# Kernel tuning notes

Hardware: AMD Instinct MI355X
Metric: run time of the kernel (lower is better)

The kernel has to match this reference:

```python
import jax, jax.numpy as jnp
import numpy as np

N = 524288
E = 16          # embedding_dim
R = 128         # dense grid resolution
H = 128         # hidden_dim
W0_SIREN = 30.0


def trilinear(grid, p):
    """grid: [R,R,R,E]; p: [N,3] in [0,1]. Returns [N,E]."""
    r = grid.shape[0]
    x = p * (r - 1)
    i0 = jnp.clip(jnp.floor(x), 0, r - 2).astype(jnp.int32)   # [N,3]
    f = x - i0.astype(x.dtype)                                # [N,3] fractional
    gf = grid.reshape(-1, grid.shape[-1])                     # [R^3, E]
    out = jnp.zeros((p.shape[0], grid.shape[-1]), dtype=grid.dtype)
    for dx in (0, 1):
        wx = f[:, 0] if dx else (1.0 - f[:, 0])
        for dy in (0, 1):
            wy = f[:, 1] if dy else (1.0 - f[:, 1])
            for dz in (0, 1):
                wz = f[:, 2] if dz else (1.0 - f[:, 2])
                idx = (i0[:, 0] + dx) * r * r + (i0[:, 1] + dy) * r + (i0[:, 2] + dz)
                out = out + gf[idx] * (wx * wy * wz)[:, None]
    return out


def siren(h, W0, b0, W1, b1, Wo, bo):
    h = jnp.sin(W0_SIREN * (h @ W0.T + b0))
    h = jnp.sin(W0_SIREN * (h @ W1.T + b1))
    return h @ Wo.T + bo   # [N,1]


def setup_inputs() -> dict:
    key = jax.random.key(0)
    ks = jax.random.split(key, 8)
    positions = jax.random.uniform(ks[0], (N, 3), dtype=jnp.float32)  # in [0,1)
    grid = jax.random.uniform(ks[1], (R, R, R, E), jnp.float32, -1e-4, 1e-4)
    din = E + 3
    c0 = float(np.sqrt(6.0 / din) / W0_SIREN)
    c1 = float(np.sqrt(6.0 / H) / W0_SIREN)
    W0 = jax.random.uniform(ks[2], (H, din), jnp.float32, -c0, c0)
    b0 = jax.random.uniform(ks[3], (H,), jnp.float32, -c0, c0)
    W1 = jax.random.uniform(ks[4], (H, H), jnp.float32, -c1, c1)
    b1 = jax.random.uniform(ks[5], (H,), jnp.float32, -c1, c1)
    Wo = jax.random.uniform(ks[6], (1, H), jnp.float32, -c1, c1)
    bo = jax.random.uniform(ks[7], (1,), jnp.float32, -c1, c1)
    return {"positions": positions, "grid": grid, "W0": W0, "b0": b0,
            "W1": W1, "b1": b1, "Wo": Wo, "bo": bo}


def reference(positions, grid, W0, b0, W1, b1, Wo, bo):
    # torch code rebinds positions = positions*0.5+0.5 BEFORE autograd.grad,
    # so the eikonal gradient is w.r.t. the transformed coordinates p.
    p = positions * 0.5 + 0.5

    def sdf_fn(pp):
        emb = trilinear(grid, pp)
        return siren(jnp.concatenate([emb, pp], axis=-1), W0, b0, W1, b1, Wo, bo)

    sdf, vjp_fn = jax.vjp(sdf_fn, p)
    (grad_x,) = vjp_fn(jnp.ones_like(sdf))
    return sdf, grad_x
```

## Files before the change

kernel.cpp:

```cpp
#include <hip/hip_runtime.h>
#include <math.h>

#define NPTS 524288
#define EDIM 16
#define RES  128
#define HDIM 128
#define DIN  19
#define OXs  (RES*RES*EDIM)
#define OYs  (RES*EDIM)
#define OZs  (EDIM)
#define NBLK 256
#define NWAVE 12
#define BATCH (NWAVE * 16)
#define NITER 11

typedef _Float16 f16;
typedef __attribute__((ext_vector_type(8))) _Float16 f16x8;
typedef __attribute__((ext_vector_type(4))) float f32x4;

#define WS_P1 0
#define WS_P2 32768
#define WS_P0 65536
#define WS_P3 73728
#define WS_T  81920
#define WS_BYTES 84992

#define DS_ORDER() asm volatile("" ::: "memory")

__global__ void pack_weights(const float* __restrict__ W0, const float* __restrict__ b0,
                             const float* __restrict__ W1, const float* __restrict__ b1,
                             const float* __restrict__ Wo, unsigned char* __restrict__ ws) {
    int idx = blockIdx.x * 256 + threadIdx.x;
    f16* p1 = (f16*)(ws + WS_P1);
    f16* p2 = (f16*)(ws + WS_P2);
    f16* p0 = (f16*)(ws + WS_P0);
    f16* p3 = (f16*)(ws + WS_P3);
    float* tb = (float*)(ws + WS_T);
    if (idx < 16384) {
        int e = idx & 7, l = (idx >> 3) & 63, t = (idx >> 9) & 3, nt = idx >> 11;
        int c = l & 15, g = l >> 4;
        p1[idx] = (f16)W1[(c + 16*nt)*HDIM + (8*g + e + 32*t)];
    } else if (idx < 32768) {
        int i = idx - 16384;
        int e = i & 7, l = (i >> 3) & 63, t = (i >> 9) & 3, nt = i >> 11;
        int c = l & 15, g = l >> 4;
        p2[i] = (f16)W1[(8*g + e + 32*t)*HDIM + (c + 16*nt)];
    } else if (idx < 36864) {
        int i = idx - 32768;
        int e = i & 7, l = (i >> 3) & 63, nt = i >> 9;
        int c = l & 15, g = l >> 4;
        int d = 8*g + e;
        p0[i] = (d < EDIM) ? (f16)W0[(c + 16*nt)*DIN + d] : (f16)0.f;
    } else if (idx < 40960) {
        int i = idx - 36864;
        int e = i & 7, l = (i >> 3) & 63, t = (i >> 9) & 3, nt = i >> 11;
        int c = l & 15, g = l >> 4;
        int din = c + 16*nt;
        p3[i] = (din < DIN) ? (f16)W0[(8*g + e + 32*t)*DIN + din] : (f16)0.f;
    } else if (idx < 41728) {
        int i = idx - 40960;
        int j = i & 127, sel = i >> 7;
        float v;
        if (sel == 0)      v = W0[j*DIN + 16];
        else if (sel == 1) v = W0[j*DIN + 17];
        else if (sel == 2) v = W0[j*DIN + 18];
        else if (sel == 3) v = b0[j];
        else if (sel == 4) v = b1[j];
        else               v = Wo[j];
        tb[i] = v;
    }
}

__global__ __launch_bounds__(768, 1)
void sdf_mfma(const float* __restrict__ pos,
              const float* __restrict__ gridp,
              const unsigned char* __restrict__ ws,
              const float* __restrict__ bo,
              float* __restrict__ out) {
    __shared__ f16 sP1[16384];
    __shared__ f16 sP2[16384];
    __shared__ f16 sP0[4096];
    __shared__ f16 sP3[4096];
    __shared__ float sT[768];
    __shared__ unsigned char sBounce[NWAVE][4352];

    const int tid = threadIdx.x;
    {
        const uint4* src = (const uint4*)ws;
        uint4* d1 = (uint4*)sP1;
        uint4* d2 = (uint4*)sP2;
        uint4* d0 = (uint4*)sP0;
        uint4* d3 = (uint4*)sP3;
        uint4* dt = (uint4*)sT;
#pragma unroll
        for (int i = 0; i < 3; ++i) {
            int k = tid + i * 768;
            if (k < 2048) { d1[k] = src[k]; d2[k] = src[2048 + k]; }
        }
        if (tid < 512) { d0[tid] = src[4096 + tid]; d3[tid] = src[4608 + tid]; }
        if (tid < 192) dt[tid] = src[5120 + tid];
    }
    __syncthreads();

    const int l = tid & 63, w = tid >> 6;
    const int c = l & 15, g = l >> 4;
    const int s = g & 1, q = g >> 1;

    f16* sBW = (f16*)sBounce[w];
    const f16x8* P0 = (const f16x8*)sP0;
    const f16x8* P1 = (const f16x8*)sP1;
    const f16x8* P2 = (const f16x8*)sP2;
    const f16x8* P3 = (const f16x8*)sP3;
    const f32x4 z4 = {0.f, 0.f, 0.f, 0.f};
    const float bov = bo[0];

#pragma unroll 1
    for (int it = 0; it < NITER; ++it) {
        const int pbase = (blockIdx.x * NITER + it) * BATCH + w * 16;
        if (pbase >= NPTS) continue;
        const int pt = pbase + c;

        const float px = fmaf(pos[3*pt+0], 0.5f, 0.5f);
        const float py = fmaf(pos[3*pt+1], 0.5f, 0.5f);
        const float pz = fmaf(pos[3*pt+2], 0.5f, 0.5f);
        const float x0 = px*127.f, x1 = py*127.f, x2 = pz*127.f;
        int i0 = (int)floorf(x0); i0 = i0 < 0 ? 0 : (i0 > 126 ? 126 : i0);
        int i1 = (int)floorf(x1); i1 = i1 < 0 ? 0 : (i1 > 126 ? 126 : i1);
        int i2 = (int)floorf(x2); i2 = i2 < 0 ? 0 : (i2 > 126 ? 126 : i2);
        const float f0 = x0 - (float)i0, f1 = x1 - (float)i1, f2 = x2 - (float)i2;
        const float wx1 = f0, wx0 = 1.f - f0;
        const float wy1 = f1, wy0 = 1.f - f1;
        const float wz1 = f2, wz0 = 1.f - f2;
        const float* gb = gridp + (size_t)((i0*RES + i1)*RES + i2)*EDIM;

        float w8[8] = {0.f,0.f,0.f,0.f,0.f,0.f,0.f,0.f};
        {
            const float wxq = q ? wx1 : wx0;
#pragma unroll
            for (int j = 0; j < 4; ++j) {
                const float* gp = gb + q*OXs + ((j>>1)&1)*OYs + (j&1)*OZs + 8*s;
                float4 qa = *(const float4*)gp;
                float4 qb = *(const float4*)(gp + 4);
                const float wc = wxq * ((j&2)?wy1:wy0) * ((j&1)?wz1:wz0);
                w8[0] = fmaf(wc, qa.x, w8[0]);  w8[1] = fmaf(wc, qa.y, w8[1]);
                w8[2] = fmaf(wc, qa.z, w8[2]);  w8[3] = fmaf(wc, qa.w, w8[3]);
                w8[4] = fmaf(wc, qb.x, w8[4]);  w8[5] = fmaf(wc, qb.y, w8[5]);
                w8[6] = fmaf(wc, qb.z, w8[6]);  w8[7] = fmaf(wc, qb.w, w8[7]);
            }
        }
        f16x8 afe;
#pragma unroll
        for (int m = 0; m < 8; ++m) {
            const float full = w8[m] + __shfl_xor(w8[m], 32);
            afe[m] = (g < 2) ? (f16)full : (f16)0.f;
        }

        f32x4 acc[8];
        __builtin_amdgcn_s_setprio(1);
#pragma unroll
        for (int nt = 0; nt < 8; ++nt)
            acc[nt] = __builtin_amdgcn_mfma_f32_16x16x32_f16(afe, P0[nt*64 + l], z4, 0, 0, 0);
        __builtin_amdgcn_s_setprio(0);

        float rpx[4], rpy[4], rpz[4];
        {
            const float* pp = pos + 3 * (pbase + 4*g);
            const float4 fa = *(const float4*)(pp + 0);
            const float4 fb = *(const float4*)(pp + 4);
            const float4 fc = *(const float4*)(pp + 8);
            rpx[0] = fmaf(fa.x, 0.5f, 0.5f); rpy[0] = fmaf(fa.y, 0.5f, 0.5f); rpz[0] = fmaf(fa.z, 0.5f, 0.5f);
            rpx[1] = fmaf(fa.w, 0.5f, 0.5f); rpy[1] = fmaf(fb.x, 0.5f, 0.5f); rpz[1] = fmaf(fb.y, 0.5f, 0.5f);
            rpx[2] = fmaf(fb.z, 0.5f, 0.5f); rpy[2] = fmaf(fb.w, 0.5f, 0.5f); rpz[2] = fmaf(fc.x, 0.5f, 0.5f);
            rpx[3] = fmaf(fc.y, 0.5f, 0.5f); rpy[3] = fmaf(fc.z, 0.5f, 0.5f); rpz[3] = fmaf(fc.w, 0.5f, 0.5f);
        }
        float t0a[8][4];
#pragma unroll
        for (int nt = 0; nt < 8; ++nt) {
            const int j = c + 16*nt;
            const float t16 = sT[j], t17 = sT[128+j], t18 = sT[256+j], tb0 = sT[384+j];
#pragma unroll
            for (int r = 0; r < 4; ++r) {
                float a0 = acc[nt][r] + tb0;
                a0 = fmaf(rpx[r], t16, a0);
                a0 = fmaf(rpy[r], t17, a0);
                a0 = fmaf(rpz[r], t18, a0);
                const float t0 = 30.f * a0;
                t0a[nt][r] = t0;
                sBW[(4*g + r)*136 + j] = (f16)__sinf(t0);
            }
        }
        DS_ORDER();

        f16x8 af[4];
#pragma unroll
        for (int t = 0; t < 4; ++t)
            af[t] = *(const f16x8*)&sBW[c*136 + 32*t + 8*g];
        __builtin_amdgcn_s_setprio(1);
#pragma unroll
        for (int nt = 0; nt < 8; ++nt) {
            f32x4 a = z4;
#pragma unroll
            for (int t = 0; t < 4; ++t)
                a = __builtin_amdgcn_mfma_f32_16x16x32_f16(af[t], P1[(nt*4+t)*64 + l], a, 0, 0, 0);
            acc[nt] = a;
        }
        __builtin_amdgcn_s_setprio(0);

        float sp[4] = {0.f, 0.f, 0.f, 0.f};
#pragma unroll
        for (int nt = 0; nt < 8; ++nt) {
            const int j = c + 16*nt;
            const float b1j = sT[512+j], woj = sT[640+j];
#pragma unroll
            for (int r = 0; r < 4; ++r) {
                const float t1 = 30.f * (acc[nt][r] + b1j);
                sp[r] = fmaf(woj, __sinf(t1), sp[r]);
                sBW[(4*g + r)*136 + j] = (f16)(30.f * woj * __cosf(t1));
            }
        }
#pragma unroll
        for (int r = 0; r < 4; ++r) {
            sp[r] += __shfl_xor(sp[r], 1);
            sp[r] += __shfl_xor(sp[r], 2);
            sp[r] += __shfl_xor(sp[r], 4);
            sp[r] += __shfl_xor(sp[r], 8);
        }
        if (c == 0) {
#pragma unroll
            for (int r = 0; r < 4; ++r) out[pbase + 4*g + r] = sp[r] + bov;
        }
        DS_ORDER();

        float4 ca[2][4];
#pragma unroll
        for (int h = 0; h < 2; ++h) {
            const int cr = 2*g + h;
            const float* gp = gb + ((cr>>2)&1)*OXs + ((cr>>1)&1)*OYs + (cr&1)*OZs;
            ca[h][0] = *(const float4*)gp;
            ca[h][1] = *(const float4*)(gp + 4);
            ca[h][2] = *(const float4*)(gp + 8);
            ca[h][3] = *(const float4*)(gp + 12);
        }

#pragma unroll
        for (int t = 0; t < 4; ++t)
            af[t] = *(const f16x8*)&sBW[c*136 + 32*t + 8*g];
        __builtin_amdgcn_s_setprio(1);
#pragma unroll
        for (int nt = 0; nt < 8; ++nt) {
            f32x4 a = z4;
#pragma unroll
            for (int t = 0; t < 4; ++t)
                a = __builtin_amdgcn_mfma_f32_16x16x32_f16(af[t], P2[(nt*4+t)*64 + l], a, 0, 0, 0);
            acc[nt] = a;
        }
        __builtin_amdgcn_s_setprio(0);

#pragma unroll
        for (int nt = 0; nt < 8; ++nt) {
            const int k = c + 16*nt;
#pragma unroll
            for (int r = 0; r < 4; ++r) {
                const float da0 = acc[nt][r] * (30.f * __cosf(t0a[nt][r]));
                sBW[(4*g + r)*136 + k] = (f16)da0;
            }
        }
        DS_ORDER();

#pragma unroll
        for (int t = 0; t < 4; ++t)
            af[t] = *(const f16x8*)&sBW[c*136 + 32*t + 8*g];
        f32x4 d3a = z4, d3b = z4;
        __builtin_amdgcn_s_setprio(1);
#pragma unroll
        for (int t = 0; t < 4; ++t) {
            d3a = __builtin_amdgcn_mfma_f32_16x16x32_f16(af[t], P3[t*64 + l],     d3a, 0, 0, 0);
            d3b = __builtin_amdgcn_mfma_f32_16x16x32_f16(af[t], P3[(4+t)*64 + l], d3b, 0, 0, 0);
        }
        __builtin_amdgcn_s_setprio(0);

        float* sDV = (float*)sBounce[w];
#pragma unroll
        for (int r = 0; r < 4; ++r) sDV[(4*g + r)*20 + c] = d3a[r];
        if (c < 3) {
#pragma unroll
            for (int r = 0; r < 4; ++r) sDV[(4*g + r)*20 + 16 + c] = d3b[r];
        }
        DS_ORDER();

        const f32x4 dva = *(const f32x4*)&sDV[c*20 + 0];
        const f32x4 dvb = *(const f32x4*)&sDV[c*20 + 4];
        const f32x4 dvc = *(const f32x4*)&sDV[c*20 + 8];
        const f32x4 dvd = *(const f32x4*)&sDV[c*20 + 12];
        float scv[2];
#pragma unroll
        for (int h = 0; h < 2; ++h) {
            float sdot = ca[h][0].x*dva[0] + ca[h][0].y*dva[1] + ca[h][0].z*dva[2] + ca[h][0].w*dva[3]
                       + ca[h][1].x*dvb[0] + ca[h][1].y*dvb[1] + ca[h][1].z*dvb[2] + ca[h][1].w*dvb[3]
                       + ca[h][2].x*dvc[0] + ca[h][2].y*dvc[1] + ca[h][2].z*dvc[2] + ca[h][2].w*dvc[3]
                       + ca[h][3].x*dvd[0] + ca[h][3].y*dvd[1] + ca[h][3].z*dvd[2] + ca[h][3].w*dvd[3];
            scv[h] = sdot;
        }
        float* sSC = (float*)sBounce[w] + 320;
        sSC[c*8 + 2*g]     = scv[0];
        sSC[c*8 + 2*g + 1] = scv[1];
        DS_ORDER();
        if (g == 0) {
            const float* scp = &sSC[c*8];
            const float sc0 = scp[0], sc1 = scp[1], sc2 = scp[2], sc3 = scp[3];
            const float sc4 = scp[4], sc5 = scp[5], sc6 = scp[6], sc7 = scp[7];
            const float gx = 127.f * (wy0*wz0*(sc4-sc0) + wy0*wz1*(sc5-sc1) +
                                      wy1*wz0*(sc6-sc2) + wy1*wz1*(sc7-sc3));
            const float gy = 127.f * (wx0*wz0*(sc2-sc0) + wx0*wz1*(sc3-sc1) +
                                      wx1*wz0*(sc6-sc4) + wx1*wz1*(sc7-sc5));
            const float gz = 127.f * (wx0*wy0*(sc1-sc0) + wx0*wy1*(sc3-sc2) +
                                      wx1*wy0*(sc5-sc4) + wx1*wy1*(sc7-sc6));
            out[NPTS + 3*pt + 0] = gx + sDV[c*20 + 16];
            out[NPTS + 3*pt + 1] = gy + sDV[c*20 + 17];
            out[NPTS + 3*pt + 2] = gz + sDV[c*20 + 18];
        }
        DS_ORDER();
    }
}

#define JCHUNK 64
__global__ void transpose_w1(const float* __restrict__ W1, float* __restrict__ W1T) {
    int idx = blockIdx.x * 256 + threadIdx.x;
    if (idx < HDIM * HDIM) {
        int j = idx >> 7, k = idx & 127;
        W1T[k * HDIM + j] = W1[j * HDIM + k];
    }
}
#define LOAD16(gq)                                   \
    float4 q0 = *(const float4*)((gq) + 0);          \
    float4 q1 = *(const float4*)((gq) + 4);          \
    float4 q2 = *(const float4*)((gq) + 8);          \
    float4 q3 = *(const float4*)((gq) + 12);

template<int RS, int CS>
__global__ __launch_bounds__(256, 2)
void sdf_fused(const float* __restrict__ pos, const float* __restrict__ gridp,
               const float* __restrict__ W0, const float* __restrict__ b0,
               const float* __restrict__ W1m, const float* __restrict__ b1,
               const float* __restrict__ Wo, const float* __restrict__ bo,
               float* __restrict__ out) {
    const int i = blockIdx.x * 256 + threadIdx.x;
    if (i >= NPTS) return;
    const float W0S = 30.0f;
    const float px = fmaf(pos[3*i+0], 0.5f, 0.5f);
    const float py = fmaf(pos[3*i+1], 0.5f, 0.5f);
    const float pz = fmaf(pos[3*i+2], 0.5f, 0.5f);
    const float x0 = px*127.f, x1 = py*127.f, x2 = pz*127.f;
    int i0 = (int)floorf(x0); i0 = i0 < 0 ? 0 : (i0 > 126 ? 126 : i0);
    int i1 = (int)floorf(x1); i1 = i1 < 0 ? 0 : (i1 > 126 ? 126 : i1);
    int i2 = (int)floorf(x2); i2 = i2 < 0 ? 0 : (i2 > 126 ? 126 : i2);
    const float f0 = x0-(float)i0, f1 = x1-(float)i1, f2 = x2-(float)i2;
    const float wx1 = f0, wx0 = 1.f-f0, wy1 = f1, wy0 = 1.f-f1, wz1 = f2, wz0 = 1.f-f2;
    const float* gb = gridp + (size_t)((i0*RES+i1)*RES+i2)*EDIM;
    float cw[8];
    cw[0]=wx0*wy0*wz0; cw[1]=wx0*wy0*wz1; cw[2]=wx0*wy1*wz0; cw[3]=wx0*wy1*wz1;
    cw[4]=wx1*wy0*wz0; cw[5]=wx1*wy0*wz1; cw[6]=wx1*wy1*wz0; cw[7]=wx1*wy1*wz1;
    float v[DIN];
#pragma unroll
    for (int e = 0; e < EDIM; ++e) v[e] = 0.f;
#pragma unroll
    for (int cr = 0; cr < 8; ++cr) {
        const float* gq = gb + ((cr>>2)&1)*OXs + ((cr>>1)&1)*OYs + (cr&1)*OZs;
        LOAD16(gq);
        const float wc = cw[cr];
        v[0]=fmaf(wc,q0.x,v[0]); v[1]=fmaf(wc,q0.y,v[1]); v[2]=fmaf(wc,q0.z,v[2]); v[3]=fmaf(wc,q0.w,v[3]);
        v[4]=fmaf(wc,q1.x,v[4]); v[5]=fmaf(wc,q1.y,v[5]); v[6]=fmaf(wc,q1.z,v[6]); v[7]=fmaf(wc,q1.w,v[7]);
        v[8]=fmaf(wc,q2.x,v[8]); v[9]=fmaf(wc,q2.y,v[9]); v[10]=fmaf(wc,q2.z,v[10]); v[11]=fmaf(wc,q2.w,v[11]);
        v[12]=fmaf(wc,q3.x,v[12]); v[13]=fmaf(wc,q3.y,v[13]); v[14]=fmaf(wc,q3.z,v[14]); v[15]=fmaf(wc,q3.w,v[15]);
    }
    v[16]=px; v[17]=py; v[18]=pz;
    float dv[DIN];
#pragma unroll
    for (int m = 0; m < DIN; ++m) dv[m] = 0.f;
    float sdf = bo[0];
#pragma unroll 1
    for (int cch = 0; cch < HDIM/JCHUNK; ++cch) {
        const int j0 = cch * JCHUNK;
        float a1c[JCHUNK];
#pragma unroll
        for (int jj = 0; jj < JCHUNK; ++jj) a1c[jj] = 0.f;
#pragma unroll 1
    for (int k = 0; k < HDIM; ++k) {
            float a0 = b0[k];
            const float* w0r = W0 + k*DIN;
#pragma unroll
            for (int m = 0; m < DIN; ++m) a0 = fmaf(w0r[m], v[m], a0);
            const float h1 = __sinf(W0S*a0);
            const float* wr = W1m + k*RS + j0*CS;
#pragma unroll
            for (int jj = 0; jj < JCHUNK; ++jj) a1c[jj] = fmaf(wr[jj*CS], h1, a1c[jj]);
        }
#pragma unroll
        for (int jj = 0; jj < JCHUNK; ++jj) {
            const float t = W0S*(a1c[jj] + b1[j0+jj]);
            float sv, co; __sincosf(t, &sv, &co);
            const float wo = Wo[j0+jj];
            sdf = fmaf(wo, sv, sdf);
            a1c[jj] = (W0S*wo)*co;
        }
#pragma unroll 1
        for (int k = 0; k < HDIM; ++k) {
            const float* wr = W1m + k*RS + j0*CS;
            float s0=0.f,s1=0.f,s2=0.f,s3=0.f;
#pragma unroll
            for (int jj = 0; jj < JCHUNK; jj += 4) {
                s0 = fmaf(wr[(jj+0)*CS], a1c[jj+0], s0);
                s1 = fmaf(wr[(jj+1)*CS], a1c[jj+1], s1);
                s2 = fmaf(wr[(jj+2)*CS], a1c[jj+2], s2);
                s3 = fmaf(wr[(jj+3)*CS], a1c[jj+3], s3);
            }
            const float dh1 = (s0+s1)+(s2+s3);
            float a0 = b0[k];
            const float* w0r = W0 + k*DIN;
#pragma unroll
            for (int m = 0; m < DIN; ++m) a0 = fmaf(w0r[m], v[m], a0);
            const float da0 = dh1 * W0S * __cosf(W0S*a0);
#pragma unroll
            for (int m = 0; m < DIN; ++m) dv[m] = fmaf(w0r[m], da0, dv[m]);
        }
    }
    float sc[8];
#pragma unroll
    for (int cr = 0; cr < 8; ++cr) {
        const float* gq = gb + ((cr>>2)&1)*OXs + ((cr>>1)&1)*OYs + (cr&1)*OZs;
        LOAD16(gq);
        float t0 = q0.x*dv[0]+q0.y*dv[1]+q0.z*dv[2]+q0.w*dv[3];
        float t1 = q1.x*dv[4]+q1.y*dv[5]+q1.z*dv[6]+q1.w*dv[7];
        float t2 = q2.x*dv[8]+q2.y*dv[9]+q2.z*dv[10]+q2.w*dv[11];
        float t3 = q3.x*dv[12]+q3.y*dv[13]+q3.z*dv[14]+q3.w*dv[15];
        sc[cr] = (t0+t1)+(t2+t3);
    }
    const float gx = 127.f*(wy0*wz0*(sc[4]-sc[0]) + wy0*wz1*(sc[5]-sc[1]) + wy1*wz0*(sc[6]-sc[2]) + wy1*wz1*(sc[7]-sc[3]));
    const float gy = 127.f*(wx0*wz0*(sc[2]-sc[0]) + wx0*wz1*(sc[3]-sc[1]) + wx1*wz0*(sc[6]-sc[4]) + wx1*wz1*(sc[7]-sc[5]));
    const float gz = 127.f*(wx0*wy0*(sc[1]-sc[0]) + wx0*wy1*(sc[3]-sc[2]) + wx1*wy0*(sc[5]-sc[4]) + wx1*wy1*(sc[7]-sc[6]));
    out[i] = sdf;
    out[NPTS + 3*i + 0] = gx + dv[16];
    out[NPTS + 3*i + 1] = gy + dv[17];
    out[NPTS + 3*i + 2] = gz + dv[18];
}

extern "C" void kernel_launch(void* const* d_in, const int* in_sizes, int n_in,
                              void* d_out, int out_size, void* d_ws, size_t ws_size,
                              hipStream_t stream) {
    const float* pos  = (const float*)d_in[0];
    const float* grid = (const float*)d_in[1];
    const float* W0   = (const float*)d_in[2];
    const float* b0   = (const float*)d_in[3];
    const float* W1   = (const float*)d_in[4];
    const float* b1   = (const float*)d_in[5];
    const float* Wo   = (const float*)d_in[6];
    const float* bo   = (const float*)d_in[7];
    float* out = (float*)d_out;

    if (ws_size >= (size_t)WS_BYTES) {
        pack_weights<<<(41728 + 255)/256, 256, 0, stream>>>(W0, b0, W1, b1, Wo, (unsigned char*)d_ws);
        sdf_mfma<<<NBLK, 768, 0, stream>>>(pos, grid, (const unsigned char*)d_ws, bo, out);
    } else if (ws_size >= (size_t)(HDIM*HDIM*sizeof(float))) {
        float* W1T = (float*)d_ws;
        transpose_w1<<<(HDIM*HDIM + 255)/256, 256, 0, stream>>>(W1, W1T);
        sdf_fused<HDIM, 1><<<NPTS/256, 256, 0, stream>>>(pos, grid, W0, b0, W1T, b1, Wo, bo, out);
    } else {
        sdf_fused<1, HDIM><<<NPTS/256, 256, 0, stream>>>(pos, grid, W0, b0, W1, b1, Wo, bo, out);
    }
}
```

Baseline: 112.3 us.

## Prefetch next iteration's positions and grid corners during backward pass

Software-pipelines the main loop. The position load, cell index computation and forward trilinear grid gathers for iteration it+1 are now issued mid-way through iteration it, after the backward-pass corner loads. The aim is to hide global-memory gather latency behind the MFMA work of the second layer and the backward pass. In exchange it holds 8 extra float4 registers plus the fractions and pointer, which raises VGPR pressure and may lower occupancy. It also loads a dummy point on the last iteration.

```diff
diff --git a/kernel.cpp b/kernel.cpp
--- a/kernel.cpp
+++ b/kernel.cpp
@@ -114,33 +114,48 @@
     const f32x4 z4 = {0.f, 0.f, 0.f, 0.f};
     const float bov = bo[0];
 
+    float cf0, cf1, cf2;
+    const float* cgb;
+    float4 cd[8];
+    {
+        const int npbase = blockIdx.x * NITER * BATCH + w * 16;
+        const int npt = (npbase < NPTS) ? npbase + c : c;
+        const float ppx = fmaf(pos[3*npt+0], 0.5f, 0.5f);
+        const float ppy = fmaf(pos[3*npt+1], 0.5f, 0.5f);
+        const float ppz = fmaf(pos[3*npt+2], 0.5f, 0.5f);
+        const float x0 = ppx*127.f, x1 = ppy*127.f, x2 = ppz*127.f;
+        int i0 = (int)floorf(x0); i0 = i0 < 0 ? 0 : (i0 > 126 ? 126 : i0);
+        int i1 = (int)floorf(x1); i1 = i1 < 0 ? 0 : (i1 > 126 ? 126 : i1);
+        int i2 = (int)floorf(x2); i2 = i2 < 0 ? 0 : (i2 > 126 ? 126 : i2);
+        cf0 = x0 - (float)i0; cf1 = x1 - (float)i1; cf2 = x2 - (float)i2;
+        cgb = gridp + (size_t)((i0*RES + i1)*RES + i2)*EDIM;
+#pragma unroll
+        for (int j = 0; j < 4; ++j) {
+            const float* gp = cgb + q*OXs + ((j>>1)&1)*OYs + (j&1)*OZs + 8*s;
+            cd[2*j]   = *(const float4*)gp;
+            cd[2*j+1] = *(const float4*)(gp + 4);
+        }
+    }
+
 #pragma unroll 1
     for (int it = 0; it < NITER; ++it) {
         const int pbase = (blockIdx.x * NITER + it) * BATCH + w * 16;
         if (pbase >= NPTS) continue;
         const int pt = pbase + c;
 
-        const float px = fmaf(pos[3*pt+0], 0.5f, 0.5f);
-        const float py = fmaf(pos[3*pt+1], 0.5f, 0.5f);
-        const float pz = fmaf(pos[3*pt+2], 0.5f, 0.5f);
-        const float x0 = px*127.f, x1 = py*127.f, x2 = pz*127.f;
-        int i0 = (int)floorf(x0); i0 = i0 < 0 ? 0 : (i0 > 126 ? 126 : i0);
-        int i1 = (int)floorf(x1); i1 = i1 < 0 ? 0 : (i1 > 126 ? 126 : i1);
-        int i2 = (int)floorf(x2); i2 = i2 < 0 ? 0 : (i2 > 126 ? 126 : i2);
-        const float f0 = x0 - (float)i0, f1 = x1 - (float)i1, f2 = x2 - (float)i2;
+        const float f0 = cf0, f1 = cf1, f2 = cf2;
         const float wx1 = f0, wx0 = 1.f - f0;
         const float wy1 = f1, wy0 = 1.f - f1;
         const float wz1 = f2, wz0 = 1.f - f2;
-        const float* gb = gridp + (size_t)((i0*RES + i1)*RES + i2)*EDIM;
+        const float* gb = cgb;
 
         float w8[8] = {0.f,0.f,0.f,0.f,0.f,0.f,0.f,0.f};
         {
             const float wxq = q ? wx1 : wx0;
 #pragma unroll
             for (int j = 0; j < 4; ++j) {
-                const float* gp = gb + q*OXs + ((j>>1)&1)*OYs + (j&1)*OZs + 8*s;
-                float4 qa = *(const float4*)gp;
-                float4 qb = *(const float4*)(gp + 4);
+                const float4 qa = cd[2*j];
+                const float4 qb = cd[2*j + 1];
                 const float wc = wxq * ((j&2)?wy1:wy0) * ((j&1)?wz1:wz0);
                 w8[0] = fmaf(wc, qa.x, w8[0]);  w8[1] = fmaf(wc, qa.y, w8[1]);
                 w8[2] = fmaf(wc, qa.z, w8[2]);  w8[3] = fmaf(wc, qa.w, w8[3]);
@@ -240,6 +255,31 @@
             ca[h][1] = *(const float4*)(gp + 4);
             ca[h][2] = *(const float4*)(gp + 8);
             ca[h][3] = *(const float4*)(gp + 12);
+        }
+
+        float nf0, nf1, nf2;
+        const float* ngbp;
+        float4 ncd[8];
+        {
+            const int npbase = pbase + BATCH * (NBLK == 0 ? 0 : 1) * 0 + (blockIdx.x * NITER + (it + 1)) * BATCH + w * 16 - pbase;
+            const int nb = (blockIdx.x * NITER + (it + 1)) * BATCH + w * 16;
+            (void)npbase;
+            const int npt = (nb < NPTS) ? nb + c : c;
+            const float ppx = fmaf(pos[3*npt+0], 0.5f, 0.5f);
+            const float ppy = fmaf(pos[3*npt+1], 0.5f, 0.5f);
+            const float ppz = fmaf(pos[3*npt+2], 0.5f, 0.5f);
+            const float x0 = ppx*127.f, x1 = ppy*127.f, x2 = ppz*127.f;
+            int i0 = (int)floorf(x0); i0 = i0 < 0 ? 0 : (i0 > 126 ? 126 : i0);
+            int i1 = (int)floorf(x1); i1 = i1 < 0 ? 0 : (i1 > 126 ? 126 : i1);
+            int i2 = (int)floorf(x2); i2 = i2 < 0 ? 0 : (i2 > 126 ? 126 : i2);
+            nf0 = x0 - (float)i0; nf1 = x1 - (float)i1; nf2 = x2 - (float)i2;
+            ngbp = gridp + (size_t)((i0*RES + i1)*RES + i2)*EDIM;
+#pragma unroll
+            for (int j = 0; j < 4; ++j) {
+                const float* gp = ngbp + q*OXs + ((j>>1)&1)*OYs + (j&1)*OZs + 8*s;
+                ncd[2*j]   = *(const float4*)gp;
+                ncd[2*j+1] = *(const float4*)(gp + 4);
+            }
         }
 
 #pragma unroll
@@ -320,6 +360,10 @@
             out[NPTS + 3*pt + 2] = gz + sDV[c*20 + 18];
         }
         DS_ORDER();
+
+        cf0 = nf0; cf1 = nf1; cf2 = nf2; cgb = ngbp;
+#pragma unroll
+        for (int j = 0; j < 8; ++j) cd[j] = ncd[j];
     }
 }
 
```

After: 162.7 us. +44.9%, slower.
